# Kernel tuning notes

Measured on AMD Instinct MI355X. Metric: run time of the kernel, lower is better.

The kernel has to match this reference:

```python
import jax, jax.numpy as jnp
import numpy as np

B, HIST, N, E = 16, 24, 256, 4096
AQI_EM, RNN_H, GNN_H, EDGE_H = 16, 64, 64, 2


def _lstm(x, W_ih, W_hh, b_ih, b_hh):
    # x: [Bn, L, in]; PyTorch LSTM cell, gate order i,f,g,o
    Bn, L, _ = x.shape
    H = W_hh.shape[1]
    xg = jnp.einsum('bli,gi->blg', x, W_ih) + b_ih  # precompute input contributions [Bn,L,4H]

    def step(carry, g_t):
        h, c = carry
        gates = g_t + h @ W_hh.T + b_hh
        i, f, g, o = jnp.split(gates, 4, axis=-1)
        c = jax.nn.sigmoid(f) * c + jax.nn.sigmoid(i) * jnp.tanh(g)
        h = jax.nn.sigmoid(o) * jnp.tanh(c)
        return (h, c), h

    init = (jnp.zeros((Bn, H), x.dtype), jnp.zeros((Bn, H), x.dtype))
    _, hs = jax.lax.scan(step, init, jnp.swapaxes(xg, 0, 1))
    return jnp.swapaxes(hs, 0, 1)  # [Bn,L,H]


def setup_inputs() -> dict:
    key = jax.random.key(0)
    ks = jax.random.split(key, 8)
    return {
        'city_aqi': jax.random.normal(ks[0], (B, HIST, N, 1), jnp.float32),
        'city_conn': jax.random.randint(ks[1], (2, E), 0, N, jnp.int32),
        'city_w': jax.random.normal(ks[2], (E, EDGE_H), jnp.float32),
        'embed_W': jax.random.normal(ks[3], (1, AQI_EM), jnp.float32) * 0.5,
        'embed_b': jnp.zeros((AQI_EM,), jnp.float32),
        'W_ih': jax.random.normal(ks[4], (4 * RNN_H, AQI_EM), jnp.float32) * (1.0 / np.sqrt(RNN_H)),
        'W_hh': jax.random.normal(ks[5], (4 * RNN_H, RNN_H), jnp.float32) * (1.0 / np.sqrt(RNN_H)),
        'b_ih': jnp.zeros((4 * RNN_H,), jnp.float32),
        'b_hh': jnp.zeros((4 * RNN_H,), jnp.float32),
        'mlp1_W': jax.random.normal(ks[6], (2 * RNN_H + EDGE_H, GNN_H), jnp.float32) * (1.0 / np.sqrt(2 * RNN_H + EDGE_H)),
        'mlp1_b': jnp.zeros((GNN_H,), jnp.float32),
        'mlp2_W': jax.random.normal(ks[7], (RNN_H + GNN_H, GNN_H), jnp.float32) * (1.0 / np.sqrt(RNN_H + GNN_H)),
        'mlp2_b': jnp.zeros((GNN_H,), jnp.float32),
        'city_num': N,
    }


def reference(city_aqi, city_conn, city_w, embed_W, embed_b, W_ih, W_hh, b_ih, b_hh, mlp1_W, mlp1_b, mlp2_W, mlp2_b, city_num):
    Bq, L, Nn, _ = city_aqi.shape
    # embedding + LSTM front-end
    x = jnp.transpose(city_aqi, (0, 2, 1, 3))          # [B,N,L,1]
    x = x @ embed_W + embed_b                          # [B,N,L,em]
    x = x.reshape(Bq * Nn, L, -1)
    h = _lstm(x, W_ih, W_hh, b_ih, b_hh)               # [B*N,L,H]
    h = jnp.transpose(h.reshape(Bq, Nn, L, -1), (0, 2, 1, 3))  # [B,L,N,H]
    # batched graph: T = B*L independent graphs with identical edge structure
    T = Bq * L
    x_flat = h.reshape(T * Nn, -1)                     # [T*N,H]
    off = jnp.arange(T, dtype=city_conn.dtype) * jnp.asarray(city_num, city_conn.dtype)
    row = (city_conn[0][None, :] + off[:, None]).reshape(-1)  # [T*E]
    col = (city_conn[1][None, :] + off[:, None]).reshape(-1)
    e = city_conn.shape[1]
    edge_attr = jnp.broadcast_to(city_w[None], (T, e, city_w.shape[1])).reshape(T * e, -1)
    # CityGNN: gather -> concat -> Linear -> scatter_mean -> concat -> Linear
    msg = jnp.concatenate([x_flat[row], x_flat[col], edge_attr], axis=1)
    msg = msg @ mlp1_W + mlp1_b                        # [T*E,gnn_h]
    agg = jax.ops.segment_sum(msg, col, num_segments=T * Nn)
    cnt = jax.ops.segment_sum(jnp.ones((T * e,), msg.dtype), col, num_segments=T * Nn)
    agg = agg / jnp.maximum(cnt, 1.0)[:, None]         # scatter_mean semantics
    out = jnp.concatenate([x_flat, agg], axis=1) @ mlp2_W + mlp2_b
    return out.reshape(-1, L, Nn, out.shape[-1])       # [B,hist_len,N,gnn_h]
```

## Files before the change

### kernel.cpp

```cpp
#include <hip/hip_runtime.h>
#include <hip/hip_bf16.h>

#define B_ 16
#define L_ 24
#define N_ 256
#define E_ 4096
#define T_ (B_ * L_)

constexpr int WP    = 0;
constexpr int WRQ   = WP + 4096;
constexpr int WRM   = WRQ + 4096;
constexpr int WBIAS = WRM + 4096;
constexpr int WALPHA= WBIAS + 16384;
constexpr int WBETA = WALPHA + 256;
constexpr int WDINV = WBETA + 256;
constexpr int WSEL  = WDINV + 256;
constexpr int WSW   = WSEL + 256;
constexpr int WCNTF = WSW + 512;
constexpr int WCOLP = WCNTF + 256;
constexpr int WROWS = WCOLP + 260;
constexpr int WHFRAG= WROWS + 4096;
constexpr int WQFRAG= WHFRAG + 8192;
constexpr int WX    = WQFRAG + 4096;
constexpr int WAFRG = WX + 3145728;

using bf16x8 = __attribute__((ext_vector_type(8))) short;
using f32x4  = __attribute__((ext_vector_type(4))) float;

__device__ __forceinline__ float sigm(float x) { return 1.f / (1.f + __expf(-x)); }
__device__ __forceinline__ float tanh_(float x) { return 2.f / (1.f + __expf(-2.f * x)) - 1.f; }
__device__ __forceinline__ unsigned f2bf(float f) {
    unsigned u = __float_as_uint(f);
    return (u + 0x7fffu + ((u >> 16) & 1u)) >> 16;
}

constexpr int HS = 72;
constexpr int NLSTM = 512;

__global__ __launch_bounds__(256, 2) void k_main(
    const float* __restrict__ aqi, const int* __restrict__ conn,
    const float* __restrict__ cw, const float* __restrict__ Wih,
    const float* __restrict__ embW, const float* __restrict__ embB,
    const float* __restrict__ bih, const float* __restrict__ bhh,
    const float* __restrict__ Whh, const float* __restrict__ m1W,
    const float* __restrict__ m1b, const float* __restrict__ m2W,
    const float* __restrict__ m2b, float* __restrict__ ws) {
    __shared__ __align__(16) char smem[65536];
    int t = threadIdx.x, blk = blockIdx.x;

    if (blk >= NLSTM) {
        int role = blk - NLSTM;
        if (role == 0) {
            int* s_cnt   = (int*)smem;
            float* s_sw0 = (float*)(smem + 1024);
            float* s_sw1 = (float*)(smem + 2048);
            float* sU    = (float*)(smem + 3072);
            s_cnt[t] = 0; s_sw0[t] = 0.f; s_sw1[t] = 0.f;
            __syncthreads();
            for (int e = t; e < E_; e += 256) {
                int c = conn[E_ + e] & 255;
                atomicAdd(&s_cnt[c], 1);
                atomicAdd(&s_sw0[c], cw[2 * e]);
                atomicAdd(&s_sw1[c], cw[2 * e + 1]);
            }
            __syncthreads();
            int cnt = s_cnt[t];
            ws[WCNTF + t] = (float)cnt;
            ws[WDINV + t] = 1.f / (float)(cnt > 1 ? cnt : 1);
            ws[WSEL + t]  = cnt > 0 ? 1.f : 0.f;
            ws[WSW + t]        = s_sw0[t];
            ws[WSW + N_ + t]   = s_sw1[t];
            if (t < 192) {
                int part = t >> 6, j = t & 63;
                float acc = 0.f;
                #pragma unroll 8
                for (int m = 0; m < 64; ++m) {
                    float w = (part == 0) ? m1W[128 * 64 + m]
                            : (part == 1) ? m1W[129 * 64 + m] : m1b[m];
                    acc = fmaf(w, m2W[(64 + m) * 64 + j], acc);
                }
                sU[part * 64 + j] = acc;
            }
            __syncthreads();
            {
                int j = t & 63;
                float u0 = sU[j], u1 = sU[64 + j], u2 = sU[128 + j];
                float b2j = m2b[j];
                int vb = t >> 6;
                #pragma unroll 8
                for (int i = 0; i < 64; ++i) {
                    int v = vb + i * 4;
                    int cv = s_cnt[v];
                    float dv = 1.f / (float)(cv > 1 ? cv : 1);
                    float bb = s_sw0[v] * u0 + s_sw1[v] * u1 + (float)cv * u2;
                    ws[WBIAS + v * 64 + j] = dv * bb + b2j;
                }
            }
            return;
        }
        if (role <= 4) {
            float* sB = (float*)smem;
            float* sM = (float*)(smem + 16384);
            int mi = role - 1;
            bool isP = mi < 2;
            int ks = mi & 1;
            #pragma unroll
            for (int i = 0; i < 16; ++i) sB[t + 256 * i] = m2W[64 * 64 + t + 256 * i];
            __syncthreads();
            int j = t & 63, kl = t >> 6;
            for (int r = 0; r < 8; ++r) {
                int kk = kl * 8 + r;
                int k = ks * 32 + kk;
                const float* arow = m1W + (isP ? k : (64 + k)) * 64;
                float acc = 0.f;
                #pragma unroll
                for (int m = 0; m < 64; m += 4) {
                    float4 a4 = *(const float4*)(arow + m);
                    acc = fmaf(a4.x, sB[m * 64 + j], acc);
                    acc = fmaf(a4.y, sB[(m + 1) * 64 + j], acc);
                    acc = fmaf(a4.z, sB[(m + 2) * 64 + j], acc);
                    acc = fmaf(a4.w, sB[(m + 3) * 64 + j], acc);
                }
                if (isP) {
                    sM[kk * 64 + j] = acc;
                } else {
                    ws[WRM + k * 64 + j] = acc;
                    sM[kk * 64 + j] = acc + m2W[k * 64 + j];
                }
            }
            __syncthreads();
            {
                int ct = t >> 6, l = t & 63;
                int fi = (isP ? 8 : 0) + ks * 4 + ct;
                int rb = (l >> 4) * 8;
                int n = ct * 16 + (l & 15);
                unsigned uu[4];
                #pragma unroll
                for (int q = 0; q < 4; ++q)
                    uu[q] = f2bf(sM[(rb + 2 * q) * 64 + n])
                          | (f2bf(sM[(rb + 2 * q + 1) * 64 + n]) << 16);
                ((uint4*)(ws + WQFRAG))[fi * 64 + l] = make_uint4(uu[0], uu[1], uu[2], uu[3]);
            }
            return;
        }
        unsigned* Mw = (unsigned*)smem;
        for (int i = t; i < 256 * 64; i += 256) Mw[i] = 0u;
        __syncthreads();
        for (int e = t; e < E_; e += 256) {
            int k = conn[e] & 255;
            int v = conn[E_ + e] & 255;
            atomicAdd(&Mw[v * 64 + (k >> 2)], 1u << ((k & 3) * 8));
        }
        __syncthreads();
        uint4* dst = (uint4*)(ws + WAFRG);
        int base = (role - 5) * 2048;
        #pragma unroll
        for (int u0 = 0; u0 < 8; ++u0) {
            int u = base + u0 * 256 + t;
            int fi = u >> 6, l = u & 63;
            int nt = fi >> 3, ks = fi & 7;
            int v = nt * 16 + (l & 15);
            int kb = ks * 8 + ((l >> 4) << 1);
            unsigned w0 = Mw[v * 64 + kb];
            unsigned w1 = Mw[v * 64 + kb + 1];
            unsigned uu[4];
            #pragma unroll
            for (int q = 0; q < 2; ++q) {
                unsigned c0 = (w0 >> (q * 16)) & 255u;
                unsigned c1 = (w0 >> (q * 16 + 8)) & 255u;
                uu[q] = f2bf((float)c0) | (f2bf((float)c1) << 16);
                unsigned d0 = (w1 >> (q * 16)) & 255u;
                unsigned d1 = (w1 >> (q * 16 + 8)) & 255u;
                uu[2 + q] = f2bf((float)d0) | (f2bf((float)d1) << 16);
            }
            dst[u] = make_uint4(uu[0], uu[1], uu[2], uu[3]);
        }
        return;
    }

    short* sHhi = (short*)smem;
    short* sHlo = (short*)(smem + 4608);
    float* sX   = (float*)(smem + 9216);
    int w = t >> 6, lane = t & 63;
    int seq0 = blk * 8;
    int b0 = seq0 >> 8, n0 = seq0 & 255;
    int c0 = lane & 15, quad = lane >> 4, q4 = quad * 4, q8 = quad * 8;
    {
        uint4* z = (uint4*)smem;
        #pragma unroll
        for (int i = 0; i < 3; ++i)
            if (t + 256 * i < 1152) z[t + 256 * i] = make_uint4(0, 0, 0, 0);
    }
    bf16x8 wreg[4][2];
    #pragma unroll
    for (int g = 0; g < 4; ++g) {
        int ct = 4 * g + w;
        #pragma unroll
        for (int ks = 0; ks < 2; ++ks) {
            const float* src = Whh + (ct * 16 + c0) * 64 + ks * 32 + q8;
            union { bf16x8 v; unsigned u[4]; } tmp;
            #pragma unroll
            for (int q = 0; q < 4; ++q)
                tmp.u[q] = f2bf(src[2 * q]) | (f2bf(src[2 * q + 1]) << 16);
            wreg[g][ks] = tmp.v;
        }
    }
    for (int i = t; i < 384; i += 256) {
        int l = i >> 4, c = i & 15;
        sX[l * 16 + c] = (c < 8) ? aqi[(b0 * L_ + l) * N_ + n0 + c] : 0.f;
    }
    float alF[4], beF[4];
    #pragma unroll
    for (int g = 0; g < 4; ++g) {
        int tp = (4 * g + w) * 16 + c0;
        float a = 0.f, b = 0.f;
        #pragma unroll
        for (int i = 0; i < 16; ++i) {
            float wv = Wih[tp * 16 + i];
            a += wv * embW[i];
            b += wv * embB[i];
        }
        alF[g] = a;
        beF[g] = b + bih[tp] + bhh[tp];
    }
    unsigned short* xws = (unsigned short*)(ws + WX);
    float cst[4] = {0.f, 0.f, 0.f, 0.f};
    bf16x8 hA[2][2] = {};
    __syncthreads();
    for (int l = 0; l < L_; ++l) {
        int buf = l & 1;
        f32x4 acc[4];
        #pragma unroll
        for (int g = 0; g < 4; ++g) {
            #pragma unroll
            for (int r = 0; r < 4; ++r)
                acc[g][r] = fmaf(sX[l * 16 + q4 + r], alF[g], beF[g]);
        }
        if (l > 0) {
            #pragma unroll
            for (int g = 0; g < 4; ++g) {
                #pragma unroll
                for (int ks = 0; ks < 2; ++ks) {
                    acc[g] = __builtin_amdgcn_mfma_f32_16x16x32_bf16(
                        hA[0][ks], wreg[g][ks], acc[g], 0, 0, 0);
                    acc[g] = __builtin_amdgcn_mfma_f32_16x16x32_bf16(
                        hA[1][ks], wreg[g][ks], acc[g], 0, 0, 0);
                }
            }
        }
        #pragma unroll
        for (int r = 0; r < 4; ++r) {
            float iv = sigm(acc[0][r]);
            float fv = sigm(acc[1][r]);
            float gv = tanh_(acc[2][r]);
            float ov = sigm(acc[3][r]);
            cst[r] = fmaf(fv, cst[r], iv * gv);
            float h = ov * tanh_(cst[r]);
            unsigned hb = f2bf(h);
            float hf = __uint_as_float(hb << 16);
            unsigned lb = f2bf(h - hf);
            sHhi[buf * (16 * HS) + (q4 + r) * HS + w * 16 + c0] = (short)hb;
            sHlo[buf * (16 * HS) + (q4 + r) * HS + w * 16 + c0] = (short)lb;
        }
        __syncthreads();
        hA[0][0] = *(const bf16x8*)&sHhi[buf * (16 * HS) + c0 * HS + q8];
        hA[0][1] = *(const bf16x8*)&sHhi[buf * (16 * HS) + c0 * HS + 32 + q8];
        hA[1][0] = *(const bf16x8*)&sHlo[buf * (16 * HS) + c0 * HS + q8];
        hA[1][1] = *(const bf16x8*)&sHlo[buf * (16 * HS) + c0 * HS + 32 + q8];
        if (t < 128) {
            int row = t >> 4, ch = t & 15;
            uint2 xa = *(const uint2*)&sHhi[buf * (16 * HS) + row * HS + ch * 4];
            *(uint2*)(xws + ((size_t)(b0 * L_ + l) * N_ + n0) * 64 + row * 64 + ch * 4) = xa;
        }
    }
}

constexpr int XS = 72;

__global__ __launch_bounds__(256, 2) void k_graph(
    const float* __restrict__ ws, float* __restrict__ out) {
    __shared__ __align__(16) short Xl[N_ * XS];
    __shared__ __align__(16) short Sl[N_ * XS];
    int tg = blockIdx.x;
    int tid = threadIdx.x;
    int lane = tid & 63, w = tid >> 6;
    int c0 = lane & 15, quad = lane >> 4, q8 = quad * 8;
    const uint4* src = (const uint4*)((const unsigned short*)(ws + WX)
                                      + (size_t)tg * (N_ * 64));
    #pragma unroll
    for (int it = 0; it < 8; ++it) {
        int idx = tid + it * 256;
        uint4 d = src[idx];
        int node = idx >> 3, q = idx & 7;
        *(uint4*)&Xl[node * XS + q * 8] = d;
    }
    float dv[16];
    #pragma unroll
    for (int nt = 0; nt < 16; ++nt) dv[nt] = ws[WDINV + nt * 16 + c0];
    __syncthreads();
    bf16x8 af[8];
    {
        int colb = w * 16 + (c0 & 14);
        int sh = (c0 & 1) * 16;
        int rbase = (lane >> 4) * 8;
        #pragma unroll
        for (int ks = 0; ks < 8; ++ks) {
            unsigned wd[8];
            #pragma unroll
            for (int j = 0; j < 8; ++j)
                wd[j] = *(const unsigned*)&Xl[(ks * 32 + rbase + j) * XS + colb];
            union { bf16x8 v; unsigned u[4]; } tmp;
            #pragma unroll
            for (int q = 0; q < 4; ++q)
                tmp.u[q] = ((wd[2 * q] >> sh) & 0xffffu)
                         | (((wd[2 * q + 1] >> sh) & 0xffffu) << 16);
            af[ks] = tmp.v;
        }
    }
    f32x4 acc[16];
    #pragma unroll
    for (int nt = 0; nt < 16; ++nt) {
        #pragma unroll
        for (int r = 0; r < 4; ++r) acc[nt][r] = 0.f;
    }
    {
        const bf16x8* bsrc = (const bf16x8*)(ws + WAFRG);
        #pragma unroll
        for (int nt = 0; nt < 16; ++nt) {
            bf16x8 bf[8];
            #pragma unroll
            for (int ks = 0; ks < 8; ++ks)
                bf[ks] = bsrc[(nt * 8 + ks) * 64 + lane];
            #pragma unroll
            for (int ks = 0; ks < 8; ++ks)
                acc[nt] = __builtin_amdgcn_mfma_f32_16x16x32_bf16(
                    af[ks], bf[ks], acc[nt], 0, 0, 0);
        }
    }
    {
        int j0 = w * 16 + quad * 4;
        #pragma unroll
        for (int nt = 0; nt < 16; ++nt) {
            float d = dv[nt];
            unsigned p0 = f2bf(acc[nt][0] * d) | (f2bf(acc[nt][1] * d) << 16);
            unsigned p1 = f2bf(acc[nt][2] * d) | (f2bf(acc[nt][3] * d) << 16);
            int v = nt * 16 + c0;
            *(uint2*)&Sl[v * XS + j0] = make_uint2(p0, p1);
        }
    }
    __syncthreads();
    bf16x8 bq[16];
    {
        const bf16x8* qf = (const bf16x8*)(ws + WQFRAG);
        #pragma unroll
        for (int i = 0; i < 16; ++i) bq[i] = qf[i * 64 + lane];
    }
    const float* bias = ws + WBIAS;
    #pragma unroll
    for (int rti = 0; rti < 4; ++rti) {
        int rt = w * 4 + rti;
        const short* xr = &Xl[(rt * 16 + c0) * XS];
        const short* sr = &Sl[(rt * 16 + c0) * XS];
        bf16x8 ax0 = *(const bf16x8*)(xr + q8);
        bf16x8 ax1 = *(const bf16x8*)(xr + 32 + q8);
        bf16x8 as0 = *(const bf16x8*)(sr + q8);
        bf16x8 as1 = *(const bf16x8*)(sr + 32 + q8);
        #pragma unroll
        for (int ct = 0; ct < 4; ++ct) {
            f32x4 a2;
            #pragma unroll
            for (int r = 0; r < 4; ++r)
                a2[r] = bias[(rt * 16 + quad * 4 + r) * 64 + ct * 16 + c0];
            a2 = __builtin_amdgcn_mfma_f32_16x16x32_bf16(ax0, bq[ct],      a2, 0, 0, 0);
            a2 = __builtin_amdgcn_mfma_f32_16x16x32_bf16(ax1, bq[4 + ct],  a2, 0, 0, 0);
            a2 = __builtin_amdgcn_mfma_f32_16x16x32_bf16(as0, bq[8 + ct],  a2, 0, 0, 0);
            a2 = __builtin_amdgcn_mfma_f32_16x16x32_bf16(as1, bq[12 + ct], a2, 0, 0, 0);
            #pragma unroll
            for (int r = 0; r < 4; ++r)
                out[((size_t)tg * 256 + rt * 16 + quad * 4 + r) * 64 + ct * 16 + c0]
                    = a2[r];
        }
    }
    int v = tid;
    float sel = ws[WSEL + v];
    if (__syncthreads_or(sel < 0.5f)) {
        if (sel < 0.5f) {
            float* og = out + ((size_t)tg * 256 + v) * 64;
            #pragma unroll
            for (int jc = 0; jc < 4; ++jc) {
                float corr[16];
                #pragma unroll
                for (int j = 0; j < 16; ++j) corr[j] = 0.f;
                #pragma unroll
                for (int k = 0; k < 64; ++k) {
                    unsigned hv = (unsigned short)Xl[v * XS + k];
                    float xk = __uint_as_float(hv << 16);
                    const float* Q = ws + WRM + k * 64 + jc * 16;
                    #pragma unroll
                    for (int j = 0; j < 16; ++j) corr[j] += xk * Q[j];
                }
                #pragma unroll
                for (int j = 0; j < 16; ++j) og[jc * 16 + j] -= corr[j];
            }
        }
    }
}

extern "C" void kernel_launch(void* const* d_in, const int* in_sizes, int n_in,
                              void* d_out, int out_size, void* d_ws, size_t ws_size,
                              hipStream_t stream) {
    const float* aqi  = (const float*)d_in[0];
    const int*   conn = (const int*)d_in[1];
    const float* cw   = (const float*)d_in[2];
    const float* embW = (const float*)d_in[3];
    const float* embB = (const float*)d_in[4];
    const float* Wih  = (const float*)d_in[5];
    const float* Whh  = (const float*)d_in[6];
    const float* bih  = (const float*)d_in[7];
    const float* bhh  = (const float*)d_in[8];
    const float* m1W  = (const float*)d_in[9];
    const float* m1b  = (const float*)d_in[10];
    const float* m2W  = (const float*)d_in[11];
    const float* m2b  = (const float*)d_in[12];
    float* ws  = (float*)d_ws;
    float* out = (float*)d_out;

    k_main<<<dim3(NLSTM + 9), dim3(256), 0, stream>>>(aqi, conn, cw, Wih, embW,
                                                      embB, bih, bhh, Whh, m1W,
                                                      m1b, m2W, m2b, ws);
    k_graph<<<dim3(T_), dim3(256), 0, stream>>>(ws, out);
}
```

Baseline: 161.0 us.

## Skip padded LSTM rows via lane shuffle and shrink shared memory for occupancy

Each LSTM block holds only 8 real sequences in a 16-row MFMA tile. The upper-half lanes now shuffle in the real rows' gate accumulators, so each lane evaluates the sigmoid/tanh cell update for 2 rows instead of 4. This halves transcendental work on the serial recurrence, and the padding rows of the h buffers are no longer written. Shared memory drops from 64 KB to 24 KB and launch bounds rise to 4 blocks per SM. To fit, each adjacency-fragment builder block now only accumulates its own quarter of destination nodes, and __syncthreads is replaced by an explicit lgkmcnt wait plus s_barrier. The risk is that hidden helper-block code could need more than the reduced shared memory.

Result: faster. 148.3 us (-7.9%).

```diff
diff --git a/kernel.cpp b/kernel.cpp
--- a/kernel.cpp
+++ b/kernel.cpp
@@ -37,7 +37,7 @@
 constexpr int HS = 72;
 constexpr int NLSTM = 512;
 
-__global__ __launch_bounds__(256, 2) void k_main(
+__global__ __launch_bounds__(256, 4) void k_main(
     const float* __restrict__ aqi, const int* __restrict__ conn,
     const float* __restrict__ cw, const float* __restrict__ Wih,
     const float* __restrict__ embW, const float* __restrict__ embB,
@@ -45,7 +45,7 @@
     const float* __restrict__ Whh, const float* __restrict__ m1W,
     const float* __restrict__ m1b, const float* __restrict__ m2W,
     const float* __restrict__ m2b, float* __restrict__ ws) {
-    __shared__ __align__(16) char smem[65536];
+    __shared__ __align__(16) char smem[24576];
     int t = threadIdx.x, blk = blockIdx.x;
 
     if (blk >= NLSTM) {
@@ -144,16 +144,18 @@
             return;
         }
         unsigned* Mw = (unsigned*)smem;
-        for (int i = t; i < 256 * 64; i += 256) Mw[i] = 0u;
+        int qd = role - 5;
+        for (int i = t; i < 64 * 64; i += 256) Mw[i] = 0u;
         __syncthreads();
         for (int e = t; e < E_; e += 256) {
             int k = conn[e] & 255;
             int v = conn[E_ + e] & 255;
-            atomicAdd(&Mw[v * 64 + (k >> 2)], 1u << ((k & 3) * 8));
+            if ((v >> 6) == qd)
+                atomicAdd(&Mw[(v & 63) * 64 + (k >> 2)], 1u << ((k & 3) * 8));
         }
         __syncthreads();
         uint4* dst = (uint4*)(ws + WAFRG);
-        int base = (role - 5) * 2048;
+        int base = qd * 2048;
         #pragma unroll
         for (int u0 = 0; u0 < 8; ++u0) {
             int u = base + u0 * 256 + t;
@@ -161,8 +163,8 @@
             int nt = fi >> 3, ks = fi & 7;
             int v = nt * 16 + (l & 15);
             int kb = ks * 8 + ((l >> 4) << 1);
-            unsigned w0 = Mw[v * 64 + kb];
-            unsigned w1 = Mw[v * 64 + kb + 1];
+            unsigned w0 = Mw[(v & 63) * 64 + kb];
+            unsigned w1 = Mw[(v & 63) * 64 + kb + 1];
             unsigned uu[4];
             #pragma unroll
             for (int q = 0; q < 2; ++q) {
@@ -185,11 +187,13 @@
     int seq0 = blk * 8;
     int b0 = seq0 >> 8, n0 = seq0 & 255;
     int c0 = lane & 15, quad = lane >> 4, q4 = quad * 4, q8 = quad * 8;
+    bool hiHalf = lane >= 32;
+    int r0 = hiHalf ? (q4 - 6) : q4;
     {
         uint4* z = (uint4*)smem;
         #pragma unroll
         for (int i = 0; i < 3; ++i)
-            if (t + 256 * i < 1152) z[t + 256 * i] = make_uint4(0, 0, 0, 0);
+            if (t + 256 * i < 576) z[t + 256 * i] = make_uint4(0, 0, 0, 0);
     }
     bf16x8 wreg[4][2];
     #pragma unroll
@@ -224,7 +228,7 @@
         beF[g] = b + bih[tp] + bhh[tp];
     }
     unsigned short* xws = (unsigned short*)(ws + WX);
-    float cst[4] = {0.f, 0.f, 0.f, 0.f};
+    float cst[2] = {0.f, 0.f};
     bf16x8 hA[2][2] = {};
     __syncthreads();
     for (int l = 0; l < L_; ++l) {
@@ -248,21 +252,31 @@
                 }
             }
         }
-        #pragma unroll
-        for (int r = 0; r < 4; ++r) {
-            float iv = sigm(acc[0][r]);
-            float fv = sigm(acc[1][r]);
-            float gv = tanh_(acc[2][r]);
-            float ov = sigm(acc[3][r]);
-            cst[r] = fmaf(fv, cst[r], iv * gv);
-            float h = ov * tanh_(cst[r]);
+        float ga[4][2];
+        #pragma unroll
+        for (int g = 0; g < 4; ++g) {
+            float v2 = __shfl_up(acc[g][2], 32);
+            float v3 = __shfl_up(acc[g][3], 32);
+            ga[g][0] = hiHalf ? v2 : acc[g][0];
+            ga[g][1] = hiHalf ? v3 : acc[g][1];
+        }
+        #pragma unroll
+        for (int rr = 0; rr < 2; ++rr) {
+            float iv = sigm(ga[0][rr]);
+            float fv = sigm(ga[1][rr]);
+            float gv = tanh_(ga[2][rr]);
+            float ov = sigm(ga[3][rr]);
+            cst[rr] = fmaf(fv, cst[rr], iv * gv);
+            float h = ov * tanh_(cst[rr]);
             unsigned hb = f2bf(h);
             float hf = __uint_as_float(hb << 16);
             unsigned lb = f2bf(h - hf);
-            sHhi[buf * (16 * HS) + (q4 + r) * HS + w * 16 + c0] = (short)hb;
-            sHlo[buf * (16 * HS) + (q4 + r) * HS + w * 16 + c0] = (short)lb;
-        }
-        __syncthreads();
+            int r = r0 + rr;
+            sHhi[buf * (16 * HS) + r * HS + w * 16 + c0] = (short)hb;
+            sHlo[buf * (16 * HS) + r * HS + w * 16 + c0] = (short)lb;
+        }
+        asm volatile("s_waitcnt lgkmcnt(0)" ::: "memory");
+        __builtin_amdgcn_s_barrier();
         hA[0][0] = *(const bf16x8*)&sHhi[buf * (16 * HS) + c0 * HS + q8];
         hA[0][1] = *(const bf16x8*)&sHhi[buf * (16 * HS) + c0 * HS + 32 + q8];
         hA[1][0] = *(const bf16x8*)&sHlo[buf * (16 * HS) + c0 * HS + q8];
```
